# Kernel tuning notes

Hardware: AMD Instinct MI355X
Metric: run time of the kernel (lower is better)

Reference implementation:

```python
import jax, jax.numpy as jnp
import numpy as np

B, S, D = 2048, 200, 128   # batch, n_steps, embedding dim per vector
H = 64                      # hidden_dim
MASK_SCALE = 1e10


def setup_inputs() -> dict:
    key = jax.random.key(0)
    ks = jax.random.split(key, 6)
    his = jax.random.normal(ks[0], (B, S, D), dtype=jnp.float32)
    target = jax.random.normal(ks[1], (B, 1, D), dtype=jnp.float32)
    # mask == 1.0 marks padded history positions (they get -1e10 added pre-softmax)
    mask = (jax.random.uniform(ks[2], (B, S)) < 0.3).astype(jnp.float32)
    W = jax.random.normal(ks[3], (3 * D, H), dtype=jnp.float32) * 0.1
    W_bias = jnp.full((H,), 0.1, dtype=jnp.float32)
    O = jax.random.normal(ks[4], (H, 1), dtype=jnp.float32) * 0.1
    O_bias = jnp.full((1,), 0.1, dtype=jnp.float32)
    return {"his": his, "target": target, "mask": mask,
            "W": W, "W_bias": W_bias, "O": O, "O_bias": O_bias}


def reference(his, target, mask, W, W_bias, O, O_bias):
    tgt = jnp.broadcast_to(target, his.shape)          # [B,S,D] tile over steps
    diff = his - tgt
    att_vec = jnp.concatenate([his, diff, tgt], axis=2)  # [B,S,3D]
    h = jax.nn.relu(jnp.einsum('bsf,fh->bsh', att_vec, W) + W_bias)  # [B,S,H]
    alpha = jnp.einsum('bsh,ho->bso', h, O) + O_bias   # [B,S,1]
    alpha = alpha[:, :, 0] - mask * MASK_SCALE         # [B,S]
    attn = jax.nn.softmax(alpha, axis=-1)              # [B,S]
    out = jnp.einsum('bs,bsd->bd', attn, his)          # weighted-sum pooling
    return out
```

## Files before the change

kernel.cpp:

```cpp
#include <hip/hip_runtime.h>

#define B_ 2048
#define S_ 200
#define D_ 128
#define H_ 64
#define MASK_SCALE 1e10f

typedef __attribute__((ext_vector_type(8))) short short8_t;
typedef __attribute__((ext_vector_type(4))) float f32x4;
typedef __attribute__((ext_vector_type(4))) unsigned short ushort4_t;

__device__ __forceinline__ unsigned short f2bf(float f) {
    unsigned u = __float_as_uint(f);
    unsigned r = (u + 0x7fffu + ((u >> 16) & 1u)) >> 16;
    return (unsigned short)r;
}
__device__ __forceinline__ float bf2f(unsigned short v) {
    return __uint_as_float(((unsigned)v) << 16);
}

__global__ __launch_bounds__(256) void prep(const float* __restrict__ W,
                                            const float* __restrict__ W_bias,
                                            const float* __restrict__ target,
                                            unsigned short* __restrict__ wfrag,
                                            float* __restrict__ tproj) {
    const int blk = blockIdx.x;
    const int t = threadIdx.x;
    if (blk < 32) {
        int idx = blk * 256 + t;
        int d = idx >> 6;
        int h = idx & 63;
        float w1 = W[d * H_ + h];
        float w2 = W[(D_ + d) * H_ + h];
        int kt = d >> 5, q = (d >> 3) & 3, j = d & 7;
        int nt = h >> 4, lm = h & 15;
        int lane = (q << 4) | lm;
        wfrag[((kt * 4 + nt) * 64 + lane) * 8 + j] = f2bf(w1 + w2);
    } else {
        int lane = t & 63, wv = t >> 6;
        int bb = (blk - 32) * 4 + wv;
        const float* tg = target + (size_t)bb * D_;
        float acc = W_bias[lane];
        #pragma unroll 4
        for (int d = 0; d < D_; ++d) {
            float w2 = W[(D_ + d) * H_ + lane];
            float w3 = W[(2 * D_ + d) * H_ + lane];
            acc = fmaf(tg[d], w3 - w2, acc);
        }
        tproj[bb * H_ + lane] = acc;
    }
}

__global__ __launch_bounds__(256, 3) void fused_kernel(const float* __restrict__ his,
                                                       const float* __restrict__ mask,
                                                       const unsigned short* __restrict__ wfrag,
                                                       const float* __restrict__ tproj,
                                                       const float* __restrict__ Ovec,
                                                       float* __restrict__ out) {
    __shared__ unsigned short hisb[S_ * D_];
    __shared__ float alpha_s[208];
    __shared__ float red8[8];
    __shared__ float tp_s[H_];
    __shared__ float ov_s[H_];
    __shared__ float pool_s[3 * D_];

    const int b    = blockIdx.x;
    const int t    = threadIdx.x;
    const int lane = t & 63;
    const int wv   = t >> 6;
    const int lm   = lane & 15;
    const int q    = lane >> 4;

    float mk = (t < S_) ? mask[(size_t)b * S_ + t] : 0.f;
    if (t < H_) {
        tp_s[t] = tproj[b * H_ + t];
        ov_s[t] = Ovec[t];
    }

    short8_t bfrag[16];
    #pragma unroll
    for (int f = 0; f < 16; ++f)
        bfrag[f] = *(const short8_t*)(wfrag + ((size_t)(f * 64 + lane)) * 8);

    const float4* hb4 = (const float4*)(his + (size_t)b * S_ * D_);
    #pragma unroll
    for (int g = 0; g < 5; ++g) {
        float4 x[5];
        #pragma unroll
        for (int j = 0; j < 5; ++j)
            x[j] = hb4[t + (g * 5 + j) * 256];
        #pragma unroll
        for (int j = 0; j < 5; ++j) {
            int i  = t + (g * 5 + j) * 256;
            int s  = i >> 5;
            int d8 = i & 31;
            int pc = (d8 >> 1) ^ (s & 15);
            ushort4_t v;
            v[0] = f2bf(x[j].x); v[1] = f2bf(x[j].y);
            v[2] = f2bf(x[j].z); v[3] = f2bf(x[j].w);
            *(ushort4_t*)((char*)hisb + s * 256 + pc * 16 + (d8 & 1) * 8) = v;
        }
    }
    __syncthreads();

    for (int tile = wv; tile < 13; tile += 4) {
        int row0 = tile * 16;
        int ar = row0 + lm; if (ar > S_ - 1) ar = S_ - 1;

        f32x4 acc[4];
        #pragma unroll
        for (int nt = 0; nt < 4; ++nt) acc[nt] = (f32x4){0.f, 0.f, 0.f, 0.f};

        #pragma unroll
        for (int kt = 0; kt < 4; ++kt) {
            int c = (kt * 4 + q) ^ (ar & 15);
            short8_t a = *(const short8_t*)((const char*)hisb + ar * 256 + c * 16);
            #pragma unroll
            for (int nt = 0; nt < 4; ++nt)
                acc[nt] = __builtin_amdgcn_mfma_f32_16x16x32_bf16(a, bfrag[kt * 4 + nt], acc[nt], 0, 0, 0);
        }

        float part[4];
        #pragma unroll
        for (int r = 0; r < 4; ++r) {
            float sum = 0.f;
            #pragma unroll
            for (int nt = 0; nt < 4; ++nt) {
                int h = nt * 16 + lm;
                float v = acc[nt][r] + tp_s[h];
                v = fmaxf(v, 0.f);
                sum = fmaf(v, ov_s[h], sum);
            }
            part[r] = sum;
        }
        #pragma unroll
        for (int off = 1; off < 16; off <<= 1) {
            #pragma unroll
            for (int r = 0; r < 4; ++r)
                part[r] += __shfl_xor(part[r], off);
        }
        if (lm == 0) {
            #pragma unroll
            for (int r = 0; r < 4; ++r)
                alpha_s[row0 + q * 4 + r] = part[r];
        }
    }
    __syncthreads();

    float a = (t < S_) ? alpha_s[t] - mk * MASK_SCALE : -INFINITY;
    float m = a;
    #pragma unroll
    for (int off = 1; off < 64; off <<= 1) m = fmaxf(m, __shfl_xor(m, off));
    if (lane == 0) red8[wv] = m;
    __syncthreads();
    m = fmaxf(fmaxf(red8[0], red8[1]), fmaxf(red8[2], red8[3]));
    float e = (t < S_) ? __expf(a - m) : 0.f;
    float ssum = e;
    #pragma unroll
    for (int off = 1; off < 64; off <<= 1) ssum += __shfl_xor(ssum, off);
    if (lane == 0) red8[4 + wv] = ssum;
    __syncthreads();
    float inv = 1.f / (red8[4] + red8[5] + red8[6] + red8[7]);
    __syncthreads();
    if (t < S_) alpha_s[t] = e * inv;
    __syncthreads();

    const int d8 = t & 31;
    const int sg = t >> 5;
    float acc0 = 0.f, acc1 = 0.f, acc2 = 0.f, acc3 = 0.f;
    #pragma unroll 5
    for (int s = sg; s < S_; s += 8) {
        float w = alpha_s[s];
        int pc = (d8 >> 1) ^ (s & 15);
        ushort4_t v = *(const ushort4_t*)((const char*)hisb + s * 256 + pc * 16 + (d8 & 1) * 8);
        acc0 = fmaf(w, bf2f(v[0]), acc0);
        acc1 = fmaf(w, bf2f(v[1]), acc1);
        acc2 = fmaf(w, bf2f(v[2]), acc2);
        acc3 = fmaf(w, bf2f(v[3]), acc3);
    }
    acc0 += __shfl_xor(acc0, 32);
    acc1 += __shfl_xor(acc1, 32);
    acc2 += __shfl_xor(acc2, 32);
    acc3 += __shfl_xor(acc3, 32);
    if (wv && lane < 32) {
        float4 p; p.x = acc0; p.y = acc1; p.z = acc2; p.w = acc3;
        *(float4*)(&pool_s[(wv - 1) * D_ + d8 * 4]) = p;
    }
    __syncthreads();
    if (wv == 0 && lane < 32) {
        #pragma unroll
        for (int k = 0; k < 3; ++k) {
            const float4 p = *(const float4*)(&pool_s[k * D_ + d8 * 4]);
            acc0 += p.x; acc1 += p.y; acc2 += p.z; acc3 += p.w;
        }
        float4 o; o.x = acc0; o.y = acc1; o.z = acc2; o.w = acc3;
        *(float4*)(out + (size_t)b * D_ + d8 * 4) = o;
    }
}

extern "C" void kernel_launch(void* const* d_in, const int* in_sizes, int n_in,
                              void* d_out, int out_size, void* d_ws, size_t ws_size,
                              hipStream_t stream) {
    const float* his    = (const float*)d_in[0];
    const float* target = (const float*)d_in[1];
    const float* mask   = (const float*)d_in[2];
    const float* W      = (const float*)d_in[3];
    const float* W_bias = (const float*)d_in[4];
    const float* Ovec   = (const float*)d_in[5];
    float* out = (float*)d_out;

    char* ws = (char*)d_ws;
    unsigned short* wfrag = (unsigned short*)ws;
    float* tproj          = (float*)(ws + 16384);

    prep<<<544, 256, 0, stream>>>(W, W_bias, target, wfrag, tproj);
    fused_kernel<<<B_, 256, 0, stream>>>(his, mask, wfrag, tproj, Ovec, out);
}
```

Before: 320.0 us.

## Fuse target projection into main kernel and use packed bf16 conversion

Moves the per-batch target projection (target·(W3−W2)+bias) out of the prep kernel and into the fused kernel. Prep now only builds the bf16 weight fragments plus a transposed W3−W2 matrix, so it launches 32 blocks instead of 544. Inside the fused kernel each wave computes a partial dot product over 32 dimensions, and the four partials are summed from shared memory after the existing barrier. The his-to-bf16 conversion now uses the v_cvt_pk_bf16_f32 instruction in place of manual rounding. This trades a large prep launch and a global round trip of tproj for extra loads of w23t (32 KB, L2-resident) in every block.

```diff
diff --git a/kernel.cpp b/kernel.cpp
--- a/kernel.cpp
+++ b/kernel.cpp
@@ -18,51 +18,42 @@
 __device__ __forceinline__ float bf2f(unsigned short v) {
     return __uint_as_float(((unsigned)v) << 16);
 }
+__device__ __forceinline__ unsigned cvt_pk_bf16(float lo, float hi) {
+    unsigned r;
+    asm("v_cvt_pk_bf16_f32 %0, %1, %2" : "=v"(r) : "v"(lo), "v"(hi));
+    return r;
+}
 
 __global__ __launch_bounds__(256) void prep(const float* __restrict__ W,
-                                            const float* __restrict__ W_bias,
-                                            const float* __restrict__ target,
                                             unsigned short* __restrict__ wfrag,
-                                            float* __restrict__ tproj) {
-    const int blk = blockIdx.x;
-    const int t = threadIdx.x;
-    if (blk < 32) {
-        int idx = blk * 256 + t;
-        int d = idx >> 6;
-        int h = idx & 63;
-        float w1 = W[d * H_ + h];
-        float w2 = W[(D_ + d) * H_ + h];
-        int kt = d >> 5, q = (d >> 3) & 3, j = d & 7;
-        int nt = h >> 4, lm = h & 15;
-        int lane = (q << 4) | lm;
-        wfrag[((kt * 4 + nt) * 64 + lane) * 8 + j] = f2bf(w1 + w2);
-    } else {
-        int lane = t & 63, wv = t >> 6;
-        int bb = (blk - 32) * 4 + wv;
-        const float* tg = target + (size_t)bb * D_;
-        float acc = W_bias[lane];
-        #pragma unroll 4
-        for (int d = 0; d < D_; ++d) {
-            float w2 = W[(D_ + d) * H_ + lane];
-            float w3 = W[(2 * D_ + d) * H_ + lane];
-            acc = fmaf(tg[d], w3 - w2, acc);
-        }
-        tproj[bb * H_ + lane] = acc;
-    }
+                                            float* __restrict__ w23t) {
+    int idx = blockIdx.x * 256 + threadIdx.x;
+    int d = idx >> 6;
+    int h = idx & 63;
+    float w1 = W[d * H_ + h];
+    float w2 = W[(D_ + d) * H_ + h];
+    float w3 = W[(2 * D_ + d) * H_ + h];
+    int kt = d >> 5, q = (d >> 3) & 3, j = d & 7;
+    int nt = h >> 4, lm = h & 15;
+    int lane = (q << 4) | lm;
+    wfrag[((kt * 4 + nt) * 64 + lane) * 8 + j] = f2bf(w1 + w2);
+    w23t[h * D_ + d] = w3 - w2;
 }
 
 __global__ __launch_bounds__(256, 3) void fused_kernel(const float* __restrict__ his,
                                                        const float* __restrict__ mask,
+                                                       const float* __restrict__ target,
+                                                       const float* __restrict__ W_bias,
                                                        const unsigned short* __restrict__ wfrag,
-                                                       const float* __restrict__ tproj,
+                                                       const float* __restrict__ w23t,
                                                        const float* __restrict__ Ovec,
                                                        float* __restrict__ out) {
     __shared__ unsigned short hisb[S_ * D_];
     __shared__ float alpha_s[208];
     __shared__ float red8[8];
-    __shared__ float tp_s[H_];
     __shared__ float ov_s[H_];
     __shared__ float pool_s[3 * D_];
+    float* tpp = pool_s;
 
     const int b    = blockIdx.x;
     const int t    = threadIdx.x;
@@ -72,9 +63,22 @@
     const int q    = lane >> 4;
 
     float mk = (t < S_) ? mask[(size_t)b * S_ + t] : 0.f;
-    if (t < H_) {
-        tp_s[t] = tproj[b * H_ + t];
-        ov_s[t] = Ovec[t];
+    if (t < H_) ov_s[t] = Ovec[t];
+
+    {
+        float acc = (wv == 0) ? W_bias[lane] : 0.f;
+        const float4* tg4 = (const float4*)(target + (size_t)b * D_) + wv * 8;
+        const float4* wt4 = (const float4*)(w23t + lane * D_) + wv * 8;
+        #pragma unroll
+        for (int i = 0; i < 8; ++i) {
+            float4 tv = tg4[i];
+            float4 wc = wt4[i];
+            acc = fmaf(tv.x, wc.x, acc);
+            acc = fmaf(tv.y, wc.y, acc);
+            acc = fmaf(tv.z, wc.z, acc);
+            acc = fmaf(tv.w, wc.w, acc);
+        }
+        tpp[wv * 64 + lane] = acc;
     }
 
     short8_t bfrag[16];
@@ -95,13 +99,20 @@
             int s  = i >> 5;
             int d8 = i & 31;
             int pc = (d8 >> 1) ^ (s & 15);
-            ushort4_t v;
-            v[0] = f2bf(x[j].x); v[1] = f2bf(x[j].y);
-            v[2] = f2bf(x[j].z); v[3] = f2bf(x[j].w);
-            *(ushort4_t*)((char*)hisb + s * 256 + pc * 16 + (d8 & 1) * 8) = v;
-        }
-    }
-    __syncthreads();
+            uint2 v;
+            v.x = cvt_pk_bf16(x[j].x, x[j].y);
+            v.y = cvt_pk_bf16(x[j].z, x[j].w);
+            *(uint2*)((char*)hisb + s * 256 + pc * 16 + (d8 & 1) * 8) = v;
+        }
+    }
+    __syncthreads();
+
+    float th[4];
+    #pragma unroll
+    for (int nt = 0; nt < 4; ++nt) {
+        int h = nt * 16 + lm;
+        th[nt] = tpp[h] + tpp[64 + h] + tpp[128 + h] + tpp[192 + h];
+    }
 
     for (int tile = wv; tile < 13; tile += 4) {
         int row0 = tile * 16;
@@ -127,7 +138,7 @@
             #pragma unroll
             for (int nt = 0; nt < 4; ++nt) {
                 int h = nt * 16 + lm;
-                float v = acc[nt][r] + tp_s[h];
+                float v = acc[nt][r] + th[nt];
                 v = fmaxf(v, 0.f);
                 sum = fmaf(v, ov_s[h], sum);
             }
@@ -211,8 +222,8 @@
 
     char* ws = (char*)d_ws;
     unsigned short* wfrag = (unsigned short*)ws;
-    float* tproj          = (float*)(ws + 16384);
-
-    prep<<<544, 256, 0, stream>>>(W, W_bias, target, wfrag, tproj);
-    fused_kernel<<<B_, 256, 0, stream>>>(his, mask, wfrag, tproj, Ovec, out);
-}
+    float* w23t           = (float*)(ws + 16384);
+
+    prep<<<32, 256, 0, stream>>>(W, wfrag, w23t);
+    fused_kernel<<<B_, 256, 0, stream>>>(his, mask, target, W_bias, wfrag, w23t, Ovec, out);
+}
```

New measurement: 313.8 us. Within noise of the previous version (-1.9%).
